# Optimization experiments

Hardware: AMD Instinct MI355X
Metric: run time of the kernel (lower is better)

Reference implementation:

```python
import jax, jax.numpy as jnp
import numpy as np

B, S, D, H, L, F = 1, 2048, 768, 12, 2, 3072
DH = D // H          # 64
W = 256              # one-sided sliding window (attention_window=512 total)
NC = S // W          # number of query chunks
VOCAB = 50265


def _ln(x, s, b, eps=1e-5):
    m = x.mean(-1, keepdims=True)
    v = ((x - m) ** 2).mean(-1, keepdims=True)
    return (x - m) / jnp.sqrt(v + eps) * s + b


def setup_inputs() -> dict:
    key = jax.random.key(0)
    ks = jax.random.split(key, 16)
    p = lambda k, sh: jax.random.normal(k, sh, jnp.float32) * 0.02
    return {
        "input_ids": jax.random.randint(ks[0], (B, S), 0, VOCAB),
        "attention_mask": jnp.ones((B, S), jnp.int32),
        "word_emb": p(ks[1], (VOCAB, D)),
        "pos_emb": p(ks[2], (S + 2, D)),          # roberta-style pos ids start at 2
        "type_emb": p(ks[3], (1, D)),
        "emb_ln_s": jnp.ones((D,), jnp.float32),
        "emb_ln_b": jnp.zeros((D,), jnp.float32),
        "Wqkv": p(ks[4], (L, 3, D, D)),
        "bqkv": jnp.zeros((L, 3, D), jnp.float32),
        "Wo": p(ks[5], (L, D, D)),
        "bo": jnp.zeros((L, D), jnp.float32),
        "ln1_s": jnp.ones((L, D), jnp.float32),
        "ln1_b": jnp.zeros((L, D), jnp.float32),
        "W1": p(ks[6], (L, D, F)),
        "b1": jnp.zeros((L, F), jnp.float32),
        "W2": p(ks[7], (L, F, D)),
        "b2": jnp.zeros((L, D), jnp.float32),
        "ln2_s": jnp.ones((L, D), jnp.float32),
        "ln2_b": jnp.zeros((L, D), jnp.float32),
        "pool_W": p(ks[8], (D, D)),
        "pool_b": jnp.zeros((D,), jnp.float32),
    }


def reference(input_ids, attention_mask, word_emb, pos_emb, type_emb,
              emb_ln_s, emb_ln_b, Wqkv, bqkv, Wo, bo, ln1_s, ln1_b,
              W1, b1, W2, b2, ln2_s, ln2_b, pool_W, pool_b):
    # ---- embeddings (roberta/longformer style) ----
    pos_ids = jnp.cumsum(attention_mask, axis=1) * attention_mask + 1  # padding_idx=1
    x = word_emb[input_ids] + pos_emb[pos_ids] + type_emb[0]
    x = _ln(x, emb_ln_s, emb_ln_b)

    # ---- banded-attention index/mask precompute (int constants) ----
    idx = jnp.arange(NC)[:, None] * W + jnp.arange(3 * W)[None, :]      # [NC, 3W] into padded seq
    rel = (jnp.arange(3 * W)[None, :] - W) - jnp.arange(W)[:, None]     # key_pos - query_pos
    band = (rel >= -W) & (rel <= W)                                      # [W, 3W]
    kmask = jnp.pad(attention_mask, ((0, 0), (W, W)))[:, idx].astype(bool)  # [B, NC, 3W]
    valid = band[None, None] & kmask[:, :, None, :]                      # [B, NC, W, 3W]

    inv_sqrt_dh = 1.0 / np.sqrt(DH)
    for l in range(L):
        qkv = jnp.einsum('bsd,tde->tbse', x, Wqkv[l]) + bqkv[l][:, None, None, :]
        q, k, v = [t.reshape(B, S, H, DH).transpose(0, 2, 1, 3) for t in qkv]  # [B,H,S,DH]
        qc = q.reshape(B, H, NC, W, DH)
        kp = jnp.pad(k, ((0, 0), (0, 0), (W, W), (0, 0)))
        vp = jnp.pad(v, ((0, 0), (0, 0), (W, W), (0, 0)))
        kc = kp[:, :, idx]                                               # [B,H,NC,3W,DH]
        vc = vp[:, :, idx]
        scores = jnp.einsum('bhcqd,bhckd->bhcqk', qc, kc) * inv_sqrt_dh  # [B,H,NC,W,3W]
        scores = jnp.where(valid[:, None], scores, -1e9)
        attn = jax.nn.softmax(scores, axis=-1)
        ctx = jnp.einsum('bhcqk,bhckd->bhcqd', attn, vc)
        ctx = ctx.reshape(B, H, S, DH).transpose(0, 2, 1, 3).reshape(B, S, D)
        x = _ln(x + ctx @ Wo[l] + bo[l], ln1_s[l], ln1_b[l])
        h = jax.nn.gelu(x @ W1[l] + b1[l], approximate=False)
        x = _ln(x + h @ W2[l] + b2[l], ln2_s[l], ln2_b[l])

    pooled = jnp.tanh(x[:, 0] @ pool_W + pool_b)
    return x, pooled
```

## Files before the change

kernel.cpp:

```cpp
#include <hip/hip_runtime.h>
#include <hip/hip_bf16.h>
#include <math.h>
#include <stddef.h>
#include <stdint.h>

typedef __hip_bfloat16 bf16;
typedef short bf16x8 __attribute__((ext_vector_type(8)));
typedef float f32x4 __attribute__((ext_vector_type(4)));

#define CS 2048
#define CD 768
#define CH 12
#define CDH 64
#define CF 3072
#define CW 256
#define CL 2
#define QKVN 2304
#define SDC ((size_t)CS * CD)
#define EPS_LD 136

__device__ __forceinline__ void gload_lds16(const bf16* g, bf16* l) {
  __builtin_amdgcn_global_load_lds(
      (const __attribute__((address_space(1))) void*)g,
      (__attribute__((address_space(3))) void*)l, 16, 0, 0);
}

__device__ __forceinline__ unsigned short f2bu(float v) {
  bf16 b = __float2bfloat16(v);
  return *(unsigned short*)&b;
}
__device__ __forceinline__ float bu2f(unsigned short u) {
  bf16 b = *(bf16*)&u;
  return __bfloat162float(b);
}

template<int NW>
__device__ __forceinline__ float block_reduce_sum(float v, float* buf) {
  #pragma unroll
  for (int off = 32; off > 0; off >>= 1) v += __shfl_down(v, off, 64);
  __syncthreads();
  if ((threadIdx.x & 63) == 0) buf[threadIdx.x >> 6] = v;
  __syncthreads();
  float s = buf[0];
  #pragma unroll
  for (int w = 1; w < NW; ++w) s += buf[w];
  return s;
}

__global__ __launch_bounds__(256) void prep_kernel(
    const float* __restrict__ Wqkv, const float* __restrict__ Wo,
    const float* __restrict__ W1, const float* __restrict__ W2,
    bf16* __restrict__ WqkvT, bf16* __restrict__ WoT,
    bf16* __restrict__ W1T, bf16* __restrict__ W2T,
    const int* __restrict__ ids, const int* __restrict__ mask,
    const float* __restrict__ wemb, const float* __restrict__ pemb,
    const float* __restrict__ temb, const float* __restrict__ gs,
    const float* __restrict__ gb, float* __restrict__ x, bf16* __restrict__ xb) {
  __shared__ float tile[64][33];
  __shared__ float red[4];
  int b = blockIdx.x;
  if (b < 6912) {
    const float* src; bf16* dst; int K, N, t;
    if (b < 1728) {
      int mat = b / 288; t = b % 288; K = 768; N = 768;
      src = Wqkv + (size_t)mat * 768 * 768; dst = WqkvT + (size_t)mat * 768 * 768;
    } else if (b < 2304) {
      b -= 1728; int mat = b / 288; t = b % 288; K = 768; N = 768;
      src = Wo + (size_t)mat * 768 * 768; dst = WoT + (size_t)mat * 768 * 768;
    } else if (b < 4608) {
      b -= 2304; int mat = b / 1152; t = b % 1152; K = 768; N = 3072;
      src = W1 + (size_t)mat * 768 * 3072; dst = W1T + (size_t)mat * 768 * 3072;
    } else {
      b -= 4608; int mat = b / 1152; t = b % 1152; K = 3072; N = 768;
      src = W2 + (size_t)mat * 3072 * 768; dst = W2T + (size_t)mat * 3072 * 768;
    }
    int nt = N / 32;
    int bn = (t % nt) * 32, bk = (t / nt) * 64;
    int tx = threadIdx.x & 31, ty = (threadIdx.x >> 5);
    #pragma unroll
    for (int i = 0; i < 8; ++i)
      tile[ty + i * 8][tx] = src[(size_t)(bk + ty + i * 8) * N + bn + tx];
    __syncthreads();
    #pragma unroll
    for (int i = 0; i < 4; ++i) {
      int n = ty + i * 8;
      if (n < 32) {
        ushort2 pk;
        pk.x = f2bu(tile[2 * tx][n]);
        pk.y = f2bu(tile[2 * tx + 1][n]);
        *(ushort2*)&dst[(size_t)(bn + n) * K + bk + 2 * tx] = pk;
      }
    }
  } else {
    int srow = b - 6912;
    int t = threadIdx.x;
    float ps = 0.f;
    for (int i = t; i <= srow; i += 256) ps += (float)mask[i];
    float tot = block_reduce_sum<4>(ps, red);
    long long pid = (long long)((int)(tot + 0.5f) * mask[srow] + 1);
    long long id = ids[srow];
    float4 v = {0.f, 0.f, 0.f, 0.f};
    if (t < 192) {
      int d = t * 4;
      float4 a = *(const float4*)&wemb[id * CD + d];
      float4 p = *(const float4*)&pemb[pid * CD + d];
      float4 tm = *(const float4*)&temb[d];
      v.x = a.x + p.x + tm.x; v.y = a.y + p.y + tm.y;
      v.z = a.z + p.z + tm.z; v.w = a.w + p.w + tm.w;
    }
    float sum = block_reduce_sum<4>(v.x + v.y + v.z + v.w, red);
    float mean = sum * (1.0f / CD);
    float cx = v.x - mean, cy = v.y - mean, cz = v.z - mean, cw = v.w - mean;
    float sqv = (t < 192) ? (cx * cx + cy * cy + cz * cz + cw * cw) : 0.f;
    float sq = block_reduce_sum<4>(sqv, red);
    float rstd = rsqrtf(sq * (1.0f / CD) + 1e-5f);
    if (t < 192) {
      int d = t * 4;
      float4 g4 = *(const float4*)&gs[d];
      float4 b4 = *(const float4*)&gb[d];
      float4 o;
      o.x = cx * rstd * g4.x + b4.x;
      o.y = cy * rstd * g4.y + b4.y;
      o.z = cz * rstd * g4.z + b4.z;
      o.w = cw * rstd * g4.w + b4.w;
      *(float4*)&x[(size_t)srow * CD + d] = o;
      ushort4 pk;
      pk.x = f2bu(o.x); pk.y = f2bu(o.y); pk.z = f2bu(o.z); pk.w = f2bu(o.w);
      *(ushort4*)&xb[(size_t)srow * CD + d] = pk;
    }
  }
}

template<int GELU, int SPLITS, int TRANS>
__device__ __forceinline__ void gemm_body(
    const bf16* __restrict__ A, const bf16* __restrict__ Bt,
    const float* __restrict__ bias, bf16* __restrict__ Cout,
    bf16* __restrict__ vTout, int M, int N, int Ktot, char* smem,
    int bx, int by) {
  bf16* As = (bf16*)smem;
  bf16* Bs = (bf16*)(smem + 64 * 64 * 2);
  bf16* eps = (bf16*)smem;
  const int tid = threadIdx.x;
  const int wave = tid >> 6, lane = tid & 63;
  const int m0 = by * 64, n0 = bx * 128;
  const int wn = wave * 64;
  const int quad = lane >> 4, rsel = lane & 15;
  const int rx = rsel & 7;
  const int r_in = lane >> 3;
  const int chunk = lane & 7;
  const int gchunk = chunk ^ r_in;
  const int Klen = Ktot / SPLITS;
  const int koff = (SPLITS > 1) ? blockIdx.z * Klen : 0;

  f32x4 acc[4][4] = {};

  for (int k0 = 0; k0 < Klen; k0 += 64) {
    #pragma unroll
    for (int i = 0; i < 12; ++i) {
      int op = wave * 12 + i;
      if (op < 8) {
        int row = op * 8 + r_in;
        gload_lds16(A + (size_t)(m0 + row) * Ktot + koff + k0 + gchunk * 8, &As[op * 512]);
      } else {
        int row = (op - 8) * 8 + r_in;
        gload_lds16(Bt + (size_t)(n0 + row) * Ktot + koff + k0 + gchunk * 8, &Bs[(op - 8) * 512]);
      }
    }
    __syncthreads();
    #pragma unroll
    for (int kh = 0; kh < 2; ++kh) {
      bf16x8 af[4], bfr[4];
      int cq = ((kh << 2) | quad);
      #pragma unroll
      for (int i = 0; i < 4; ++i)
        af[i] = *(const bf16x8*)&As[(i * 16 + rsel) * 64 + (cq ^ rx) * 8];
      #pragma unroll
      for (int j = 0; j < 4; ++j)
        bfr[j] = *(const bf16x8*)&Bs[(wn + j * 16 + rsel) * 64 + (cq ^ rx) * 8];
      #pragma unroll
      for (int i = 0; i < 4; ++i)
        #pragma unroll
        for (int j = 0; j < 4; ++j) {
          if (TRANS)
            acc[i][j] = __builtin_amdgcn_mfma_f32_16x16x32_bf16(af[i], bfr[j], acc[i][j], 0, 0, 0);
          else
            acc[i][j] = __builtin_amdgcn_mfma_f32_16x16x32_bf16(bfr[j], af[i], acc[i][j], 0, 0, 0);
        }
    }
    __syncthreads();
  }

  if (!TRANS) {
    #pragma unroll
    for (int j = 0; j < 4; ++j) {
      int cb = wn + j * 16 + quad * 4;
      float4 bv = {0.f, 0.f, 0.f, 0.f};
      if (SPLITS == 1 || blockIdx.z == 0) bv = *(const float4*)&bias[n0 + cb];
      #pragma unroll
      for (int i = 0; i < 4; ++i) {
        float v0 = acc[i][j][0] + bv.x;
        float v1 = acc[i][j][1] + bv.y;
        float v2 = acc[i][j][2] + bv.z;
        float v3 = acc[i][j][3] + bv.w;
        if (GELU) {
          v0 = 0.5f * v0 * (1.0f + erff(v0 * 0.70710678118654752f));
          v1 = 0.5f * v1 * (1.0f + erff(v1 * 0.70710678118654752f));
          v2 = 0.5f * v2 * (1.0f + erff(v2 * 0.70710678118654752f));
          v3 = 0.5f * v3 * (1.0f + erff(v3 * 0.70710678118654752f));
        }
        ushort4 pk;
        pk.x = f2bu(v0); pk.y = f2bu(v1); pk.z = f2bu(v2); pk.w = f2bu(v3);
        *(ushort4*)&eps[(i * 16 + rsel) * EPS_LD + cb] = pk;
      }
    }
    __syncthreads();
    const size_t zb = (SPLITS > 1) ? (size_t)blockIdx.z * M * N : 0;
    #pragma unroll
    for (int it = 0; it < 8; ++it) {
      int row = it * 8 + (tid >> 4);
      int c = tid & 15;
      bf16x8 v = *(const bf16x8*)&eps[row * EPS_LD + c * 8];
      *(bf16x8*)&Cout[zb + (size_t)(m0 + row) * N + n0 + c * 8] = v;
    }
  } else {
    #pragma unroll
    for (int j = 0; j < 4; ++j) {
      float bv = bias[n0 + wn + j * 16 + rsel];
      #pragma unroll
      for (int i = 0; i < 4; ++i) {
        ushort4 pk;
        pk.x = f2bu(acc[i][j][0] + bv);
        pk.y = f2bu(acc[i][j][1] + bv);
        pk.z = f2bu(acc[i][j][2] + bv);
        pk.w = f2bu(acc[i][j][3] + bv);
        *(ushort4*)&eps[(wn + j * 16 + rsel) * 72 + i * 16 + quad * 4] = pk;
      }
    }
    __syncthreads();
    #pragma unroll
    for (int it = 0; it < 8; ++it) {
      int row = it * 16 + (tid >> 3);
      int c = tid & 7;
      bf16x8 v = *(const bf16x8*)&eps[row * 72 + c * 8];
      *(bf16x8*)&vTout[(size_t)(n0 - 1536 + row) * CS + m0 + c * 8] = v;
    }
  }
}

template<int GELU, int SPLITS, int VTFUSE>
__global__ __launch_bounds__(128, 3) void gemm_mfma(
    const bf16* __restrict__ A, const bf16* __restrict__ Bt,
    const float* __restrict__ bias, bf16* __restrict__ Cout,
    bf16* __restrict__ vTout, int M, int N, int Ktot) {
  __shared__ __align__(16) char smem[24576];
  int nx = gridDim.x, ny = gridDim.y;
  int nwg = nx * ny;
  int orig = blockIdx.x + blockIdx.y * nx;
  int bx, by;
  if (nwg & 7) { bx = blockIdx.x; by = blockIdx.y; }
  else {
    int q8 = nwg >> 3;
    int nid = (orig & 7) * q8 + (orig >> 3);
    bx = nid / ny; by = nid - bx * ny;
  }
  if (VTFUSE && bx * 128 >= 1536)
    gemm_body<0, 1, 1>(A, Bt, bias, Cout, vTout, M, N, Ktot, smem, bx, by);
  else
    gemm_body<GELU, SPLITS, 0>(A, Bt, bias, Cout, vTout, M, N, Ktot, smem, bx, by);
}

__global__ __launch_bounds__(256) void attn_mfma(
    const bf16* __restrict__ qkv, const bf16* __restrict__ vT,
    const int* __restrict__ mask, bf16* __restrict__ ctx) {
  __shared__ __align__(16) bf16 Ks[64 * 64];
  __shared__ __align__(16) bf16 Vs[64 * 64];
  __shared__ __align__(16) bf16 Ps[4][16][72];
  const int h = blockIdx.y;
  const int q0 = blockIdx.x * 64;
  const int tid = threadIdx.x;
  const int wv = tid >> 6, lane = tid & 63;
  const int quad = lane >> 4, rsel = lane & 15;
  const int rx = rsel & 7;
  const int qw = q0 + wv * 16;
  const int r_in = lane >> 3, chunk = lane & 7, gchunk = chunk ^ r_in;

  const bf16* qp = &qkv[(size_t)(qw + rsel) * QKVN + h * CDH + quad * 8];
  bf16x8 qf0 = *(const bf16x8*)qp;
  bf16x8 qf1 = *(const bf16x8*)(qp + 32);

  float mi[4], li[4];
  f32x4 o[4] = {};
  #pragma unroll
  for (int r = 0; r < 4; ++r) { mi[r] = -1e30f; li[r] = 0.f; }

  #pragma unroll 1
  for (int kt = 0; kt < 9; ++kt) {
    int kbase = q0 - CW + kt * 64;
    bool tile_in = (kbase + 63 >= 0) && (kbase < CS);
    if (tile_in) {
      #pragma unroll
      for (int i = 0; i < 4; ++i) {
        int op = wv * 4 + i;
        if (op < 8) {
          int krow = min(max(kbase + op * 8 + r_in, 0), CS - 1);
          gload_lds16(&qkv[(size_t)krow * QKVN + 768 + h * CDH + gchunk * 8], &Ks[op * 512]);
        } else {
          int vop = op - 8;
          int kc = min(max(kbase + gchunk * 8, 0), CS - 8);
          gload_lds16(&vT[(size_t)(h * CDH + vop * 8 + r_in) * CS + kc], &Vs[vop * 512]);
        }
      }
    }
    __syncthreads();
    bool active = tile_in && (kbase + 63 >= qw - CW) && (kbase <= qw + 15 + CW);
    if (active) {
      f32x4 sc[4];
      #pragma unroll
      for (int nt = 0; nt < 4; ++nt) {
        const bf16* kp = &Ks[(nt * 16 + rsel) * 64];
        bf16x8 kf0 = *(const bf16x8*)(kp + (quad ^ rx) * 8);
        bf16x8 kf1 = *(const bf16x8*)(kp + ((quad + 4) ^ rx) * 8);
        f32x4 z = {};
        __builtin_amdgcn_s_setprio(1);
        z = __builtin_amdgcn_mfma_f32_16x16x32_bf16(qf0, kf0, z, 0, 0, 0);
        z = __builtin_amdgcn_mfma_f32_16x16x32_bf16(qf1, kf1, z, 0, 0, 0);
        __builtin_amdgcn_s_setprio(0);
        sc[nt] = z;
      }
      float mx[4] = {-1e30f, -1e30f, -1e30f, -1e30f};
      #pragma unroll
      for (int nt = 0; nt < 4; ++nt) {
        int pp = kbase + nt * 16 + rsel;
        int ppc = min(max(pp, 0), CS - 1);
        bool kvld = (pp >= 0) && (pp < CS) && (mask[ppc] != 0);
        #pragma unroll
        for (int r = 0; r < 4; ++r) {
          int qr = qw + quad * 4 + r;
          float s = sc[nt][r] * 0.125f;
          bool band = (pp >= qr - CW) && (pp <= qr + CW);
          s = (kvld && band) ? s : -1e9f;
          sc[nt][r] = s;
          mx[r] = fmaxf(mx[r], s);
        }
      }
      #pragma unroll
      for (int r = 0; r < 4; ++r) {
        #pragma unroll
        for (int off = 1; off < 16; off <<= 1)
          mx[r] = fmaxf(mx[r], __shfl_xor(mx[r], off, 64));
      }
      float al[4], rs[4] = {};
      #pragma unroll
      for (int r = 0; r < 4; ++r) {
        float mn = fmaxf(mi[r], mx[r]);
        al[r] = __expf(mi[r] - mn);
        mi[r] = mn;
      }
      #pragma unroll
      for (int nt = 0; nt < 4; ++nt)
        #pragma unroll
        for (int r = 0; r < 4; ++r) {
          float p = __expf(sc[nt][r] - mi[r]);
          sc[nt][r] = p;
          rs[r] += p;
        }
      #pragma unroll
      for (int r = 0; r < 4; ++r) {
        #pragma unroll
        for (int off = 1; off < 16; off <<= 1)
          rs[r] += __shfl_xor(rs[r], off, 64);
        li[r] = li[r] * al[r] + rs[r];
      }
      #pragma unroll
      for (int d = 0; d < 4; ++d)
        #pragma unroll
        for (int r = 0; r < 4; ++r) o[d][r] *= al[r];
      #pragma unroll
      for (int nt = 0; nt < 4; ++nt)
        #pragma unroll
        for (int r = 0; r < 4; ++r)
          Ps[wv][quad * 4 + r][nt * 16 + rsel] = __float2bfloat16(sc[nt][r]);
      __asm__ volatile("s_waitcnt lgkmcnt(0)" ::: "memory");
      __builtin_amdgcn_sched_barrier(0);
      bf16x8 pf0 = *(const bf16x8*)&Ps[wv][rsel][quad * 8];
      bf16x8 pf1 = *(const bf16x8*)&Ps[wv][rsel][32 + quad * 8];
      #pragma unroll
      for (int d = 0; d < 4; ++d) {
        const bf16* vr = &Vs[(d * 16 + rsel) * 64];
        bf16x8 vf0 = *(const bf16x8*)(vr + (quad ^ rx) * 8);
        bf16x8 vf1 = *(const bf16x8*)(vr + ((quad + 4) ^ rx) * 8);
        __builtin_amdgcn_s_setprio(1);
        o[d] = __builtin_amdgcn_mfma_f32_16x16x32_bf16(pf0, vf0, o[d], 0, 0, 0);
        o[d] = __builtin_amdgcn_mfma_f32_16x16x32_bf16(pf1, vf1, o[d], 0, 0, 0);
        __builtin_amdgcn_s_setprio(0);
      }
    }
    __syncthreads();
  }

  float inv[4];
  #pragma unroll
  for (int r = 0; r < 4; ++r) inv[r] = 1.0f / li[r];
  #pragma unroll
  for (int d = 0; d < 4; ++d)
    #pragma unroll
    for (int r = 0; r < 4; ++r)
      Ps[wv][quad * 4 + r][d * 16 + rsel] = __float2bfloat16(o[d][r] * inv[r]);
  __asm__ volatile("s_waitcnt lgkmcnt(0)" ::: "memory");
  __builtin_amdgcn_sched_barrier(0);
  #pragma unroll
  for (int it = 0; it < 2; ++it) {
    int row = it * 8 + (lane >> 3);
    bf16x8 vv = *(const bf16x8*)&Ps[wv][row][(lane & 7) * 8];
    *(bf16x8*)&ctx[(size_t)(qw + row) * CD + h * CDH + (lane & 7) * 8] = vv;
  }
}

template<int P>
__global__ __launch_bounds__(192) void add_ln_kernel(
    const bf16* __restrict__ g, const float* __restrict__ xin,
    float* __restrict__ xout, bf16* __restrict__ xb,
    const float* __restrict__ gs, const float* __restrict__ gb) {
  __shared__ float red[3];
  int srow = blockIdx.x;
  int d = threadIdx.x * 4;
  size_t base = (size_t)srow * CD + d;
  float4 a = *(const float4*)&xin[base];
  #pragma unroll
  for (int p = 0; p < P; ++p) {
    ushort4 gg = *(const ushort4*)&g[p * SDC + base];
    a.x += bu2f(gg.x); a.y += bu2f(gg.y); a.z += bu2f(gg.z); a.w += bu2f(gg.w);
  }
  float sum = block_reduce_sum<3>(a.x + a.y + a.z + a.w, red);
  float mean = sum * (1.0f / CD);
  float cx = a.x - mean, cy = a.y - mean, cz = a.z - mean, cw = a.w - mean;
  float sq = block_reduce_sum<3>(cx * cx + cy * cy + cz * cz + cw * cw, red);
  float rstd = rsqrtf(sq * (1.0f / CD) + 1e-5f);
  float4 g4 = *(const float4*)&gs[d];
  float4 b4 = *(const float4*)&gb[d];
  float4 o;
  o.x = cx * rstd * g4.x + b4.x;
  o.y = cy * rstd * g4.y + b4.y;
  o.z = cz * rstd * g4.z + b4.z;
  o.w = cw * rstd * g4.w + b4.w;
  *(float4*)&xout[base] = o;
  ushort4 pk;
  pk.x = f2bu(o.x); pk.y = f2bu(o.y); pk.z = f2bu(o.z); pk.w = f2bu(o.w);
  *(ushort4*)&xb[base] = pk;
}

__global__ __launch_bounds__(256) void pool_kernel(
    const float* __restrict__ x, const float* __restrict__ Wp,
    const float* __restrict__ bp, float* __restrict__ out) {
  __shared__ float xs[CD];
  __shared__ float red[4][64];
  int t = threadIdx.x;
  for (int i = t; i < CD; i += 256) xs[i] = x[i];
  __syncthreads();
  int n = blockIdx.x * 64 + (t & 63);
  int kp = t >> 6;
  float acc = 0.f;
  #pragma unroll 4
  for (int kk = kp * 192; kk < kp * 192 + 192; ++kk)
    acc = fmaf(xs[kk], Wp[(size_t)kk * CD + n], acc);
  red[kp][t & 63] = acc;
  __syncthreads();
  if (t < 64) {
    int nn = blockIdx.x * 64 + t;
    out[nn] = tanhf(red[0][t] + red[1][t] + red[2][t] + red[3][t] + bp[nn]);
  }
}

extern "C" void kernel_launch(void* const* d_in, const int* in_sizes, int n_in,
                              void* d_out, int out_size, void* d_ws, size_t ws_size,
                              hipStream_t stream) {
  const int*   ids   = (const int*)d_in[0];
  const int*   mask  = (const int*)d_in[1];
  const float* wemb  = (const float*)d_in[2];
  const float* pemb  = (const float*)d_in[3];
  const float* temb  = (const float*)d_in[4];
  const float* elns  = (const float*)d_in[5];
  const float* elnb  = (const float*)d_in[6];
  const float* Wqkv  = (const float*)d_in[7];
  const float* bqkv  = (const float*)d_in[8];
  const float* Wo    = (const float*)d_in[9];
  const float* bo    = (const float*)d_in[10];
  const float* ln1s  = (const float*)d_in[11];
  const float* ln1b  = (const float*)d_in[12];
  const float* W1    = (const float*)d_in[13];
  const float* b1    = (const float*)d_in[14];
  const float* W2    = (const float*)d_in[15];
  const float* b2    = (const float*)d_in[16];
  const float* ln2s  = (const float*)d_in[17];
  const float* ln2b  = (const float*)d_in[18];
  const float* poolW = (const float*)d_in[19];
  const float* poolb = (const float*)d_in[20];

  const size_t SD = SDC;
  const size_t SF = (size_t)CS * CF;

  char* w = (char*)d_ws;
  float* x    = (float*)w; w += SD * 4;
  bf16*  xb   = (bf16*)w;  w += SD * 2;
  bf16*  qkv  = (bf16*)w;  w += (size_t)CS * QKVN * 2;
  bf16*  vT   = (bf16*)w;  w += SD * 2;
  bf16*  ctxb = (bf16*)w;  w += SD * 2;
  bf16*  t1b  = (bf16*)w;  w += SF * 2;
  bf16*  t2   = (bf16*)w;  w += SD * 2 * 4;
  bf16* WqkvT = (bf16*)w;  w += (size_t)CL * QKVN * CD * 2;
  bf16* WoT   = (bf16*)w;  w += (size_t)CL * CD * CD * 2;
  bf16* W1T   = (bf16*)w;  w += (size_t)CL * CF * CD * 2;
  bf16* W2T   = (bf16*)w;  w += (size_t)CL * CD * CF * 2;

  prep_kernel<<<6912 + CS, 256, 0, stream>>>(
      Wqkv, Wo, W1, W2, WqkvT, WoT, W1T, W2T,
      ids, mask, wemb, pemb, temb, elns, elnb, x, xb);

  for (int l = 0; l < CL; ++l) {
    gemm_mfma<0,1,1><<<dim3(QKVN/128, CS/64), 128, 0, stream>>>(
        xb, WqkvT + (size_t)l * QKVN * CD, bqkv + (size_t)l * 3 * CD, qkv, vT, CS, QKVN, CD);
    attn_mfma<<<dim3(CS/64, CH), 256, 0, stream>>>(qkv, vT, mask, ctxb);
    gemm_mfma<0,2,0><<<dim3(CD/128, CS/64, 2), 128, 0, stream>>>(
        ctxb, WoT + (size_t)l * CD * CD, bo + (size_t)l * CD, t2, nullptr, CS, CD, CD);
    add_ln_kernel<2><<<CS, 192, 0, stream>>>(t2, x, x, xb,
        ln1s + (size_t)l * CD, ln1b + (size_t)l * CD);
    gemm_mfma<1,1,0><<<dim3(CF/128, CS/64), 128, 0, stream>>>(
        xb, W1T + (size_t)l * CF * CD, b1 + (size_t)l * CF, t1b, nullptr, CS, CF, CD);
    gemm_mfma<0,2,0><<<dim3(CD/128, CS/64, 2), 128, 0, stream>>>(
        t1b, W2T + (size_t)l * CD * CF, b2 + (size_t)l * CD, t2, nullptr, CS, CD, CF);
    float* lastx = (l == CL - 1) ? (float*)d_out : x;
    add_ln_kernel<2><<<CS, 192, 0, stream>>>(t2, x, lastx, xb,
        ln2s + (size_t)l * CD, ln2b + (size_t)l * CD);
  }

  pool_kernel<<<12, 256, 0, stream>>>((float*)d_out, poolW, poolb, (float*)d_out + SD);
}
```

Measured before the change: 531.3 us.

## Double-buffer GEMM LDS tiles to overlap global loads with MFMA

Restructures the GEMM main loop into a two-stage software pipeline. The next K tile is loaded into a second LDS buffer while MFMAs run on the current one, and each iteration ends with a single wait-and-barrier. The goal is to hide global-to-LDS load latency behind compute. In exchange, LDS use per block doubles to 48 KB, which may reduce how many blocks fit per CU under the launch bound of 3.

```diff
diff --git a/kernel.cpp b/kernel.cpp
--- a/kernel.cpp
+++ b/kernel.cpp
@@ -138,7 +138,7 @@
     bf16* __restrict__ vTout, int M, int N, int Ktot, char* smem,
     int bx, int by) {
   bf16* As = (bf16*)smem;
-  bf16* Bs = (bf16*)(smem + 64 * 64 * 2);
+  bf16* Bs = (bf16*)(smem + 16384);
   bf16* eps = (bf16*)smem;
   const int tid = threadIdx.x;
   const int wave = tid >> 6, lane = tid & 63;
@@ -151,32 +151,48 @@
   const int gchunk = chunk ^ r_in;
   const int Klen = Ktot / SPLITS;
   const int koff = (SPLITS > 1) ? blockIdx.z * Klen : 0;
+  const int nt = Klen / 64;
 
   f32x4 acc[4][4] = {};
 
-  for (int k0 = 0; k0 < Klen; k0 += 64) {
+  auto STAGE = [&](int buf, int t) {
+    const int kk = koff + t * 64;
+    bf16* Asb = As + buf * 4096;
+    bf16* Bsb = Bs + buf * 8192;
     #pragma unroll
     for (int i = 0; i < 12; ++i) {
       int op = wave * 12 + i;
       if (op < 8) {
         int row = op * 8 + r_in;
-        gload_lds16(A + (size_t)(m0 + row) * Ktot + koff + k0 + gchunk * 8, &As[op * 512]);
+        gload_lds16(A + (size_t)(m0 + row) * Ktot + kk + gchunk * 8, &Asb[op * 512]);
       } else {
         int row = (op - 8) * 8 + r_in;
-        gload_lds16(Bt + (size_t)(n0 + row) * Ktot + koff + k0 + gchunk * 8, &Bs[(op - 8) * 512]);
-      }
-    }
-    __syncthreads();
+        gload_lds16(Bt + (size_t)(n0 + row) * Ktot + kk + gchunk * 8, &Bsb[(op - 8) * 512]);
+      }
+    }
+  };
+
+  STAGE(0, 0);
+  __asm__ volatile("s_waitcnt vmcnt(0)" ::: "memory");
+  __builtin_amdgcn_s_barrier();
+  __builtin_amdgcn_sched_barrier(0);
+
+  int cur = 0;
+  for (int t = 0; t < nt; ++t) {
+    if (t + 1 < nt) STAGE(cur ^ 1, t + 1);
+    __builtin_amdgcn_sched_barrier(0);
+    const bf16* Asb = As + cur * 4096;
+    const bf16* Bsb = Bs + cur * 8192;
     #pragma unroll
     for (int kh = 0; kh < 2; ++kh) {
       bf16x8 af[4], bfr[4];
       int cq = ((kh << 2) | quad);
       #pragma unroll
       for (int i = 0; i < 4; ++i)
-        af[i] = *(const bf16x8*)&As[(i * 16 + rsel) * 64 + (cq ^ rx) * 8];
+        af[i] = *(const bf16x8*)&Asb[(i * 16 + rsel) * 64 + (cq ^ rx) * 8];
       #pragma unroll
       for (int j = 0; j < 4; ++j)
-        bfr[j] = *(const bf16x8*)&Bs[(wn + j * 16 + rsel) * 64 + (cq ^ rx) * 8];
+        bfr[j] = *(const bf16x8*)&Bsb[(wn + j * 16 + rsel) * 64 + (cq ^ rx) * 8];
       #pragma unroll
       for (int i = 0; i < 4; ++i)
         #pragma unroll
@@ -187,7 +203,10 @@
             acc[i][j] = __builtin_amdgcn_mfma_f32_16x16x32_bf16(bfr[j], af[i], acc[i][j], 0, 0, 0);
         }
     }
-    __syncthreads();
+    __asm__ volatile("s_waitcnt vmcnt(0)" ::: "memory");
+    __builtin_amdgcn_s_barrier();
+    __builtin_amdgcn_sched_barrier(0);
+    cur ^= 1;
   }
 
   if (!TRANS) {
@@ -252,7 +271,7 @@
     const bf16* __restrict__ A, const bf16* __restrict__ Bt,
     const float* __restrict__ bias, bf16* __restrict__ Cout,
     bf16* __restrict__ vTout, int M, int N, int Ktot) {
-  __shared__ __align__(16) char smem[24576];
+  __shared__ __align__(16) char smem[49152];
   int nx = gridDim.x, ny = gridDim.y;
   int nwg = nx * ny;
   int orig = blockIdx.x + blockIdx.y * nx;
```

After: 512.6 us. 1.04x faster.
